# Performance work log

Measured on AMD Instinct MI355X. Metric: run time of the kernel, lower is better.

## Reference

```python
import jax, jax.numpy as jnp
import numpy as np
from jax import lax

NUM_MASK_PARAMS = 67  # 66 weights (64 feat + 2 coord channels) + 1 bias
NUM_GEN_PARAMS = 134


def _coord_maps(h, w, dtype):
    yy = jnp.broadcast_to(jnp.linspace(-1.0, 1.0, h, dtype=dtype)[:, None], (h, w))
    xx = jnp.broadcast_to(jnp.linspace(-1.0, 1.0, w, dtype=dtype)[None, :], (h, w))
    return xx, yy


def _dynamic_head(x_cat, p):
    # x_cat: [66, H, W]; p: [num_ins, 67] -> [num_ins, H, W]
    w = p[:, :NUM_MASK_PARAMS - 1]
    b = p[:, NUM_MASK_PARAMS - 1]
    return jnp.einsum('ic,chw->ihw', w, x_cat) + b[:, None, None]


def setup_inputs() -> dict:
    key = jax.random.key(0)
    ks = jax.random.split(key, 10)
    C, HM, WM, HH, WH, MB, HID = 256, 272, 480, 136, 240, 64, 64
    rn = lambda k, s, sc=1.0: jax.random.normal(k, s, dtype=jnp.float32) * sc
    return {
        'out0': rn(ks[0], (1, C, HM, WM)),
        'out1': rn(ks[1], (1, C, HH, WH)),
        'hm_w': rn(ks[2], (1, C), 0.05),
        'hm_b': jnp.zeros((1,), jnp.float32),
        'params_w': rn(ks[3], (NUM_GEN_PARAMS, C), 0.05),
        'params_b': rn(ks[4], (NUM_GEN_PARAMS,), 0.05),
        'mb_w': rn(ks[5], (MB, C, 3, 3), 0.05),
        'mb_b': jnp.zeros((MB,), jnp.float32),
        'mlp_w1': rn(ks[6], (HM, HID), 0.05),
        'mlp_b1': jnp.zeros((HID,), jnp.float32),
        'mlp_w2': rn(ks[7], (HID, 2), 0.05),
        'mlp_b2': jnp.zeros((2,), jnp.float32),
        'num_ins': 4,
    }


def reference(out0, out1, hm_w, hm_b, params_w, params_b, mb_w, mb_b,
              mlp_w1, mlp_b1, mlp_w2, mlp_b2, num_ins):
    h_mask, w_mask = out0.shape[2], out0.shape[3]
    h_hm, w_hm = out1.shape[2], out1.shape[3]

    # ctnet head: 1x1 convs on the stride-16 feature
    hm = jnp.einsum('kc,bchw->bkhw', hm_w, out1) + hm_b[None, :, None, None]
    params = jnp.einsum('kc,bchw->bkhw', params_w, out1) + params_b[None, :, None, None]
    hm = jnp.clip(jax.nn.sigmoid(hm), 1e-4, 1.0 - 1e-4)  # [1,1,h_hm,w_hm]
    # [1,134,h,w] -> [h*w, 134]
    params_flat = jnp.transpose(params[0], (1, 2, 0)).reshape(-1, NUM_GEN_PARAMS)

    # 3x3 maxpool NMS (stride 1, pad 1), keep only local peaks
    hmax = lax.reduce_window(hm, -jnp.inf, lax.max, (1, 1, 3, 3), (1, 1, 1, 1),
                             [(0, 0), (0, 0), (1, 1), (1, 1)])
    keep = (hmax == hm).astype(hm.dtype)
    heat_nms = (hm * keep).reshape(-1)

    scores, inds = lax.top_k(heat_nms, num_ins)

    # mask branch: 3x3 conv + relu on the stride-8 feature
    mask_branch = lax.conv_general_dilated(out0, mb_w, (1, 1), 'SAME',
                                           dimension_numbers=('NCHW', 'OIHW', 'NCHW'))
    mask_branch = jax.nn.relu(mask_branch + mb_b[None, :, None, None])  # [1,64,H,W]

    xx, yy = _coord_maps(h_mask, w_mask, mask_branch.dtype)
    x_cat = jnp.concatenate([mask_branch[0], xx[None], yy[None]], axis=0)  # [66,H,W]

    gen_params = params_flat[inds]  # [num_ins, 134]
    masks0 = _dynamic_head(x_cat, gen_params[:, :NUM_MASK_PARAMS])   # [num_ins,H,W]
    regs0 = _dynamic_head(x_cat, gen_params[:, NUM_MASK_PARAMS:])    # [num_ins,H,W]

    # row-wise vertical-range MLP over h_mask
    feat_range = jnp.transpose(masks0, (0, 2, 1))  # [num_ins, w_mask, h_mask]
    h1 = jax.nn.relu(feat_range @ mlp_w1 + mlp_b1)
    feat_range = h1 @ mlp_w2 + mlp_b2  # [num_ins, w_mask, 2]

    return scores, inds, regs0, masks0, feat_range
```

## Files before the change

### kernel.cpp

```cpp
#include <hip/hip_runtime.h>
#include <math.h>
#include <limits.h>

#define C_IN 256
#define HM_H 136
#define HM_W 240
#define HM_N (HM_H * HM_W)
#define MB   64
#define MH   272
#define MW   480
#define MN   (MH * MW)
#define NP   134
#define NI   4
#define HID  64

#define REG_OFF   8
#define MASK_OFF  (8 + NI * MN)
#define FEAT_OFF  (8 + 2 * NI * MN)

#define WS_HM   0
#define WS_CV   HM_N
#define WS_CI   (HM_N + 512)
#define WS_GP   (2 * HM_N)
#define WS_WT_F 65824

typedef float  f32x4  __attribute__((ext_vector_type(4)));
typedef short  bf16x8 __attribute__((ext_vector_type(8)));
typedef unsigned short u16x8 __attribute__((ext_vector_type(8)));

__device__ __forceinline__ unsigned short f2bf(float f) {
  unsigned int u = __float_as_uint(f);
  u += 0x7FFFu + ((u >> 16) & 1u);
  return (unsigned short)(u >> 16);
}
__device__ __forceinline__ float b2f(unsigned short h) {
  return __uint_as_float(((unsigned int)h) << 16);
}

__device__ __forceinline__ void glds16(const void* g, void* l) {
  __builtin_amdgcn_global_load_lds(
      (const __attribute__((address_space(1))) unsigned int*)g,
      (__attribute__((address_space(3))) unsigned int*)l, 16, 0, 0);
}

__global__ void k_prep(const float* __restrict__ mb_w, unsigned short* __restrict__ wt,
                       const float* __restrict__ out1, const float* __restrict__ hm_w,
                       const float* __restrict__ hm_b, float* __restrict__ ws_hm) {
  __shared__ float part[4][64];
  if (blockIdx.x < 576) {
    int idx = blockIdx.x * 256 + threadIdx.x;
    int j    = idx & 7;
    int lane = (idx >> 3) & 63;
    int nt   = (idx >> 9) & 3;
    int gt   = idx >> 11;
    int t    = gt % 9;
    int g    = gt / 9;
    int n = nt * 16 + (lane & 15);
    int c = g * 32 + (lane >> 4) * 8 + j;
    wt[idx] = f2bf(mb_w[(n * C_IN + c) * 9 + t]);
  } else {
    int b = blockIdx.x - 576, t = threadIdx.x;
    int cg = t >> 6, pl = t & 63;
    int p = b * 64 + pl;
    float s = 0.f;
    #pragma unroll 16
    for (int c = 0; c < 64; ++c)
      s += hm_w[cg * 64 + c] * out1[(cg * 64 + c) * HM_N + p];
    part[cg][pl] = s;
    __syncthreads();
    if (t < 64) {
      float tot = part[0][t] + part[1][t] + part[2][t] + part[3][t] + hm_b[0];
      float sig = 1.f / (1.f + expf(-tot));
      sig = fminf(fmaxf(sig, 1e-4f), 1.f - 1e-4f);
      ws_hm[b * 64 + t] = sig;
    }
  }
}

__device__ __forceinline__ bool better(float av, int ai, float bv, int bi) {
  return (av > bv) || (av == bv && ai < bi);
}

template<int NTHR>
__device__ void top4_tree(float* sv, int* si, int t) {
  for (int s = NTHR / 2; s >= 1; s >>= 1) {
    if (t < s) {
      float a[4], b[4]; int ai[4], bj[4];
      #pragma unroll
      for (int k = 0; k < 4; ++k) {
        a[k] = sv[t * 4 + k];        ai[k] = si[t * 4 + k];
        b[k] = sv[(t + s) * 4 + k];  bj[k] = si[(t + s) * 4 + k];
      }
      float ov[4]; int oi[4];
      int i = 0, j = 0;
      #pragma unroll
      for (int k = 0; k < 4; ++k) {
        if (better(a[i], ai[i], b[j], bj[j])) { ov[k] = a[i]; oi[k] = ai[i]; ++i; }
        else                                   { ov[k] = b[j]; oi[k] = bj[j]; ++j; }
      }
      #pragma unroll
      for (int k = 0; k < 4; ++k) { sv[t * 4 + k] = ov[k]; si[t * 4 + k] = oi[k]; }
    }
    __syncthreads();
  }
}

__global__ void k_nms_top(const float* __restrict__ ws_hm, float* __restrict__ candv,
                          int* __restrict__ candi) {
  __shared__ float sv[256 * 4];
  __shared__ int   si[256 * 4];
  int b = blockIdx.x, t = threadIdx.x;
  float v = -1.f; int idx = INT_MAX;
  if (t < 255) {
    int p = b * 255 + t;
    int y = p / HM_W, x = p - y * HM_W;
    float c = ws_hm[p], m = c;
    #pragma unroll
    for (int dy = -1; dy <= 1; ++dy)
      #pragma unroll
      for (int dx = -1; dx <= 1; ++dx) {
        int yy = y + dy, xx = x + dx;
        if (yy >= 0 && yy < HM_H && xx >= 0 && xx < HM_W)
          m = fmaxf(m, ws_hm[yy * HM_W + xx]);
      }
    v = (c == m) ? c : 0.f;
    idx = p;
  }
  sv[t * 4] = v; si[t * 4] = idx;
  #pragma unroll
  for (int k = 1; k < 4; ++k) { sv[t * 4 + k] = -1.f; si[t * 4 + k] = INT_MAX; }
  __syncthreads();
  top4_tree<256>(sv, si, t);
  if (t == 0) {
    #pragma unroll
    for (int k = 0; k < 4; ++k) { candv[b * 4 + k] = sv[k]; candi[b * 4 + k] = si[k]; }
  }
}

__global__ void k_gen(const float* __restrict__ candv, const int* __restrict__ candi,
                      const float* __restrict__ out1, const float* __restrict__ params_w,
                      const float* __restrict__ params_b, float* __restrict__ ws_gp,
                      float* __restrict__ d_out) {
  __shared__ float sv[128 * 4];
  __shared__ int   si[128 * 4];
  __shared__ float col[C_IN];
  int t = threadIdx.x, i = blockIdx.x;
  if (t < 128) {
    #pragma unroll
    for (int k = 0; k < 4; ++k) { sv[t * 4 + k] = candv[t * 4 + k]; si[t * 4 + k] = candi[t * 4 + k]; }
  }
  __syncthreads();
  top4_tree<128>(sv, si, t);
  if (i == 0 && t < 4) {
    d_out[t]     = sv[t];
    d_out[4 + t] = (float)si[t];
  }
  int p = si[i];
  col[t] = out1[t * HM_N + p];
  __syncthreads();
  if (t < NP) {
    float s = params_b[t];
    #pragma unroll 8
    for (int c = 0; c < C_IN; ++c) s += params_w[t * C_IN + c] * col[c];
    ws_gp[i * NP + t] = s;
  }
}

#define SR   18
#define RP   36
#define BUFU (SR * RP * 32)
#define WOFF (2 * BUFU)

#define PIPE_BARRIER() do {                                   \
    __builtin_amdgcn_sched_barrier(0);                        \
    asm volatile("s_waitcnt lgkmcnt(0)" ::: "memory");        \
    __builtin_amdgcn_s_barrier();                             \
    __builtin_amdgcn_sched_barrier(0);                        \
  } while (0)

#define STAGE_W3(G, B)                                                    \
  if (wv == 7 && (G) < 24) {                                              \
    const char* wsrc = (const char*)wt + (G) * 12288 + lane * 16;         \
    char* wdst = (char*)smem + 2 * WOFF + (B) * 12288;                    \
    _Pragma("unroll")                                                     \
    for (int i_ = 0; i_ < 12; ++i_)                                       \
      glds16(wsrc + i_ * 1024, wdst + i_ * 1024);                         \
  }

#define MFMA16(A, B, C) __builtin_amdgcn_mfma_f32_16x16x32_bf16(A, B, C, 0, 0, 0)

#define TAPS3(P) {                                                        \
    const unsigned short* wl = smem + WOFF + (P) * 6144 + lane * 8;       \
    _Pragma("unroll")                                                     \
    for (int tt = 0; tt < 3; ++tt) {                                      \
      bf16x8 bb0 = *(const bf16x8*)(wl + tt * 2048);                      \
      bf16x8 bb1 = *(const bf16x8*)(wl + tt * 2048 + 512);                \
      bf16x8 bb2 = *(const bf16x8*)(wl + tt * 2048 + 1024);               \
      bf16x8 bb3 = *(const bf16x8*)(wl + tt * 2048 + 1536);               \
      unsigned pk = lrdp[(P) * 3 + tt];                                   \
      const unsigned short* c0 = cur + (pk & 0xFFFFu);                    \
      const unsigned short* c1 = cur + (pk >> 16);                        \
      bf16x8 a0 = *(const bf16x8*)c0;                                     \
      bf16x8 a1 = *(const bf16x8*)(c0 + 512);                             \
      bf16x8 a2 = *(const bf16x8*)c1;                                     \
      bf16x8 a3 = *(const bf16x8*)(c1 + 512);                             \
      acc[0][0] = MFMA16(a0, bb0, acc[0][0]);                             \
      acc[0][1] = MFMA16(a0, bb1, acc[0][1]);                             \
      acc[0][2] = MFMA16(a0, bb2, acc[0][2]);                             \
      acc[0][3] = MFMA16(a0, bb3, acc[0][3]);                             \
      acc[1][0] = MFMA16(a1, bb0, acc[1][0]);                             \
      acc[1][1] = MFMA16(a1, bb1, acc[1][1]);                             \
      acc[1][2] = MFMA16(a1, bb2, acc[1][2]);                             \
      acc[1][3] = MFMA16(a1, bb3, acc[1][3]);                             \
      acc[2][0] = MFMA16(a2, bb0, acc[2][0]);                             \
      acc[2][1] = MFMA16(a2, bb1, acc[2][1]);                             \
      acc[2][2] = MFMA16(a2, bb2, acc[2][2]);                             \
      acc[2][3] = MFMA16(a2, bb3, acc[2][3]);                             \
      acc[3][0] = MFMA16(a3, bb0, acc[3][0]);                             \
      acc[3][1] = MFMA16(a3, bb1, acc[3][1]);                             \
      acc[3][2] = MFMA16(a3, bb2, acc[3][2]);                             \
      acc[3][3] = MFMA16(a3, bb3, acc[3][3]);                             \
    } }

__device__ __forceinline__ void stage_store8(unsigned short* buf, const f32x4* dq,
                                             bool gv, const int* lw, unsigned sm) {
  #pragma unroll
  for (int e = 0; e < 4; ++e) if ((sm >> e) & 1u) {
    u16x8 v;
    #pragma unroll
    for (int j = 0; j < 8; ++j) v[j] = f2bf(gv ? dq[j][e] : 0.f);
    *(u16x8*)(buf + lw[e]) = v;
  }
}

__global__ __launch_bounds__(512, 2) void k_conv_mfma(
    const float* __restrict__ out0, const unsigned short* __restrict__ wt,
    const float* __restrict__ mb_b, const float* __restrict__ ws_gp,
    float* __restrict__ d_out) {
  __shared__ unsigned short smem[2 * BUFU + 3 * 6144];

  int tid  = threadIdx.x;
  int lane = tid & 63;
  int wv   = tid >> 6;
  int n15  = lane & 15;
  int kq   = lane >> 4;
  int gx0 = blockIdx.x * 32, gy0 = blockIdx.y * 16;

  bool ustage = tid < 360;
  int u    = ustage ? tid : 0;
  int co8  = u / 180;
  int rem  = u - co8 * 180;
  int row  = rem / 10;
  int qx   = rem - row * 10;
  int iy   = gy0 + row - 1;
  int ixq  = gx0 + 4 * qx - 4;
  bool gvld = ustage && (iy >= 0) && (iy < MH) && (ixq >= 0) && (ixq + 3 < MW);
  int goffA = gvld ? (co8 * 8 * MN + iy * MW + ixq) : 0;
  int lwsA[4]; unsigned smask = 0;
  #pragma unroll
  for (int e = 0; e < 4; ++e) {
    int sx = 4 * qx - 3 + e;
    bool sv = ustage && (sx >= 0) && (sx < RP);
    int pixw = row * RP + (sv ? sx : 0);
    int w2 = (pixw ^ (pixw >> 2)) & 3;
    int q  = (pixw ^ row) & 1;
    lwsA[e] = (pixw >> 1) * 64 + ((co8 ^ w2) << 4) + q * 8;
    if (sv) smask |= (1u << e);
  }

  unsigned lrdp[9];
  #pragma unroll
  for (int t = 0; t < 9; ++t) {
    int ty = t / 3, tx = t - ty * 3;
    int sr0 = 2 * wv + ty;
    int pix0 = sr0 * RP + n15 + tx;
    int w20 = (pix0 ^ (pix0 >> 2)) & 3;
    int q0  = (pix0 ^ sr0) & 1;
    unsigned o0 = (pix0 >> 1) * 64 + ((kq ^ w20) << 4) + q0 * 8;
    int sr1 = sr0 + 1;
    int pix1 = sr1 * RP + n15 + tx;
    int w21 = (pix1 ^ (pix1 >> 2)) & 3;
    int q1  = (pix1 ^ sr1) & 1;
    unsigned o1 = (pix1 >> 1) * 64 + ((kq ^ w21) << 4) + q1 * 8;
    lrdp[t] = o0 | (o1 << 16);
  }

  {
    f32x4 dq[8];
    if (ustage) {
      const float* sp = out0 + goffA;
      #pragma unroll
      for (int j = 0; j < 8; ++j) dq[j] = *(const f32x4*)(sp + j * MN);
    }
    stage_store8(smem, dq, gvld, lwsA, smask);
    if (ustage) {
      const float* sp = out0 + goffA + 16 * MN;
      #pragma unroll
      for (int j = 0; j < 8; ++j) dq[j] = *(const f32x4*)(sp + j * MN);
    }
    {
      int lwsB[4];
      #pragma unroll
      for (int e = 0; e < 4; ++e) lwsB[e] = lwsA[e] ^ 32;
      stage_store8(smem, dq, gvld, lwsB, smask);
    }
  }
  __builtin_amdgcn_sched_barrier(0);
  STAGE_W3(0, 0);
  STAGE_W3(1, 1);
  if (wv == 7) asm volatile("s_waitcnt vmcnt(12)" ::: "memory");
  PIPE_BARRIER();

  f32x4 acc[4][4];
  #pragma unroll
  for (int i = 0; i < 4; ++i)
    #pragma unroll
    for (int nt = 0; nt < 4; ++nt)
      acc[i][nt] = (f32x4){0.f, 0.f, 0.f, 0.f};

  #pragma unroll 1
  for (int g = 0; g < 8; ++g) {
    const unsigned short* cur = smem + (g & 1) * BUFU;
    unsigned short*       nxt = smem + ((g + 1) & 1) * BUFU;
    const float*          src = out0 + (g + 1) * (32 * MN);
    f32x4 dq[8];

    STAGE_W3(3 * g + 2, 2);
    if (g < 7 && ustage) {
      const float* sp = src + goffA;
      #pragma unroll
      for (int j = 0; j < 8; ++j) dq[j] = *(const f32x4*)(sp + j * MN);
    }
    __builtin_amdgcn_sched_barrier(0);
    TAPS3(0)
    if (wv == 7) asm volatile("s_waitcnt vmcnt(12)" ::: "memory");
    PIPE_BARRIER();

    STAGE_W3(3 * g + 3, 0);
    if (g < 7) stage_store8(nxt, dq, gvld, lwsA, smask);
    if (g < 7 && ustage) {
      const float* sp = src + goffA + 16 * MN;
      #pragma unroll
      for (int j = 0; j < 8; ++j) dq[j] = *(const f32x4*)(sp + j * MN);
    }
    __builtin_amdgcn_sched_barrier(0);
    TAPS3(1)
    if (wv == 7) {
      if (g == 7) asm volatile("s_waitcnt vmcnt(0)" ::: "memory");
      else        asm volatile("s_waitcnt vmcnt(12)" ::: "memory");
    }
    PIPE_BARRIER();

    STAGE_W3(3 * g + 4, 1);
    if (g < 7) {
      int lwsB[4];
      #pragma unroll
      for (int e = 0; e < 4; ++e) lwsB[e] = lwsA[e] ^ 32;
      stage_store8(nxt, dq, gvld, lwsB, smask);
    }
    __builtin_amdgcn_sched_barrier(0);
    TAPS3(2)
    if (wv == 7) {
      if (g == 7) asm volatile("s_waitcnt vmcnt(0)" ::: "memory");
      else        asm volatile("s_waitcnt vmcnt(12)" ::: "memory");
    }
    PIPE_BARRIER();
  }

  #define ES 66
  {
    float bias[4];
    #pragma unroll
    for (int nt = 0; nt < 4; ++nt) bias[nt] = mb_b[nt * 16 + n15];
    #pragma unroll
    for (int i = 0; i < 4; ++i) {
      int pbase = (2 * wv + (i >> 1)) * 32 + (i & 1) * 16;
      #pragma unroll
      for (int nt = 0; nt < 4; ++nt)
        #pragma unroll
        for (int reg = 0; reg < 4; ++reg) {
          float vv = fmaxf(acc[i][nt][reg] + bias[nt], 0.f);
          smem[(pbase + kq * 4 + reg) * ES + nt * 16 + n15] = f2bf(vv);
        }
    }
  }
  __syncthreads();

  int p = tid & 255, hh = tid >> 8;
  int ob = hh * 32;
  float* pf = (float*)smem + 16896;
  #pragma unroll 1
  for (int ps = 0; ps < 2; ++ps) {
    int pixel = ps * 256 + p;
    float mres[4] = {0.f, 0.f, 0.f, 0.f};
    float rres[4] = {0.f, 0.f, 0.f, 0.f};
    #pragma unroll 8
    for (int o = 0; o < 32; ++o) {
      float v = b2f(smem[pixel * ES + ob + o]);
      #pragma unroll
      for (int i = 0; i < 4; ++i) {
        mres[i] += ws_gp[i * NP + ob + o] * v;
        rres[i] += ws_gp[i * NP + 67 + ob + o] * v;
      }
    }
    if (hh) {
      #pragma unroll
      for (int i = 0; i < 4; ++i) { pf[p * 8 + i] = mres[i]; pf[p * 8 + 4 + i] = rres[i]; }
    }
    __syncthreads();
    if (!hh) {
      int r = pixel >> 5, xcol = pixel & 31;
      int gy = gy0 + r, gx = gx0 + xcol;
      float xc = -1.f + (2.f / 479.f) * (float)gx;
      float yc = -1.f + (2.f / 271.f) * (float)gy;
      int pix = gy * MW + gx;
      #pragma unroll
      for (int i = 0; i < 4; ++i) {
        const float* gp = ws_gp + i * NP;
        d_out[MASK_OFF + i * MN + pix] = mres[i] + pf[p * 8 + i]     + gp[66]  + gp[64]  * xc + gp[65]  * yc;
        d_out[REG_OFF  + i * MN + pix] = rres[i] + pf[p * 8 + 4 + i] + gp[133] + gp[131] * xc + gp[132] * yc;
      }
    }
    __syncthreads();
  }
}

__global__ void k_mlp(const float* __restrict__ masks0, const float* __restrict__ w1,
                      const float* __restrict__ b1, const float* __restrict__ w2,
                      const float* __restrict__ b2, float* __restrict__ d_out) {
  int blk = blockIdx.x;
  int i = blk / MW;
  int w = blk - i * MW;
  int k = threadIdx.x;
  const float* mcol = masks0 + i * MN + w;
  float s = b1[k];
  #pragma unroll 4
  for (int h = 0; h < MH; ++h) s += mcol[h * MW] * w1[h * HID + k];
  s = fmaxf(s, 0.f);
  float o0 = s * w2[k * 2 + 0];
  float o1 = s * w2[k * 2 + 1];
  #pragma unroll
  for (int off = 32; off >= 1; off >>= 1) {
    o0 += __shfl_down(o0, off);
    o1 += __shfl_down(o1, off);
  }
  if (k == 0) {
    d_out[FEAT_OFF + blk * 2 + 0] = o0 + b2[0];
    d_out[FEAT_OFF + blk * 2 + 1] = o1 + b2[1];
  }
}

extern "C" void kernel_launch(void* const* d_in, const int* in_sizes, int n_in,
                              void* d_out, int out_size, void* d_ws, size_t ws_size,
                              hipStream_t stream) {
  const float* out0     = (const float*)d_in[0];
  const float* out1     = (const float*)d_in[1];
  const float* hm_w     = (const float*)d_in[2];
  const float* hm_b     = (const float*)d_in[3];
  const float* params_w = (const float*)d_in[4];
  const float* params_b = (const float*)d_in[5];
  const float* mb_w     = (const float*)d_in[6];
  const float* mb_b     = (const float*)d_in[7];
  const float* mlp_w1   = (const float*)d_in[8];
  const float* mlp_b1   = (const float*)d_in[9];
  const float* mlp_w2   = (const float*)d_in[10];
  const float* mlp_b2   = (const float*)d_in[11];

  float* ws      = (float*)d_ws;
  float* ws_hm   = ws + WS_HM;
  float* candv   = ws + WS_CV;
  int*   candi   = (int*)(ws + WS_CI);
  float* ws_gp   = ws + WS_GP;
  unsigned short* ws_wt = (unsigned short*)(ws + WS_WT_F);
  float* out     = (float*)d_out;

  k_prep<<<1086, 256, 0, stream>>>(mb_w, ws_wt, out1, hm_w, hm_b, ws_hm);
  k_nms_top<<<128, 256, 0, stream>>>(ws_hm, candv, candi);
  k_gen<<<NI, 256, 0, stream>>>(candv, candi, out1, params_w, params_b, ws_gp, out);
  dim3 gconv(MW / 32, MH / 16);
  k_conv_mfma<<<gconv, 512, 0, stream>>>(out0, ws_wt, mb_b, ws_gp, out);
  k_mlp<<<NI * MW, 64, 0, stream>>>(out + MASK_OFF, mlp_w1, mlp_b1, mlp_w2, mlp_b2, out);
}
```

Before: 311.6 us.

## Deepen conv input prefetch to two groups and remap blocks across XCDs

The 3x3 conv kernel now keeps two register sets (dqA/dqB) and prefetches input channels one full group ahead, issuing global loads a whole iteration before the LDS store instead of within the same iteration. This is meant to hide more global-load latency behind the MFMA taps. The 2D grid also becomes a 1D grid of 255 blocks, remapped so that consecutive tiles land on the same XCD (L2 locality for the halo rows). The extra registers may hurt occupancy under launch_bounds(512,2), and the vmcnt waits were not adjusted for the deeper pipeline.

```diff
diff --git a/kernel.cpp b/kernel.cpp
--- a/kernel.cpp
+++ b/kernel.cpp
@@ -244,7 +244,12 @@
   int wv   = tid >> 6;
   int n15  = lane & 15;
   int kq   = lane >> 4;
-  int gx0 = blockIdx.x * 32, gy0 = blockIdx.y * 16;
+
+  int orig = blockIdx.x;
+  int xcd  = orig & 7, pos = orig >> 3;
+  int wgid = (xcd < 7) ? (xcd * 32 + pos) : (224 + pos);
+  int bx = wgid / 17, by = wgid - bx * 17;
+  int gx0 = bx * 32, gy0 = by * 16;
 
   bool ustage = tid < 360;
   int u    = ustage ? tid : 0;
@@ -285,25 +290,32 @@
     lrdp[t] = o0 | (o1 << 16);
   }
 
+  f32x4 dqA[8], dqB[8];
+  if (ustage) {
+    const float* sp = out0 + goffA;
+    #pragma unroll
+    for (int j = 0; j < 8; ++j) dqA[j] = *(const f32x4*)(sp + j * MN);
+  }
+  stage_store8(smem, dqA, gvld, lwsA, smask);
+  if (ustage) {
+    const float* sp = out0 + goffA + 16 * MN;
+    #pragma unroll
+    for (int j = 0; j < 8; ++j) dqB[j] = *(const f32x4*)(sp + j * MN);
+  }
   {
-    f32x4 dq[8];
-    if (ustage) {
-      const float* sp = out0 + goffA;
-      #pragma unroll
-      for (int j = 0; j < 8; ++j) dq[j] = *(const f32x4*)(sp + j * MN);
-    }
-    stage_store8(smem, dq, gvld, lwsA, smask);
-    if (ustage) {
-      const float* sp = out0 + goffA + 16 * MN;
-      #pragma unroll
-      for (int j = 0; j < 8; ++j) dq[j] = *(const f32x4*)(sp + j * MN);
-    }
-    {
-      int lwsB[4];
-      #pragma unroll
-      for (int e = 0; e < 4; ++e) lwsB[e] = lwsA[e] ^ 32;
-      stage_store8(smem, dq, gvld, lwsB, smask);
-    }
+    int lwsB[4];
+    #pragma unroll
+    for (int e = 0; e < 4; ++e) lwsB[e] = lwsA[e] ^ 32;
+    stage_store8(smem, dqB, gvld, lwsB, smask);
+  }
+  __builtin_amdgcn_sched_barrier(0);
+  if (ustage) {
+    const float* sp = out0 + 32 * MN + goffA;
+    #pragma unroll
+    for (int j = 0; j < 8; ++j) dqA[j] = *(const f32x4*)(sp + j * MN);
+    const float* sq = out0 + 32 * MN + goffA + 16 * MN;
+    #pragma unroll
+    for (int j = 0; j < 8; ++j) dqB[j] = *(const f32x4*)(sq + j * MN);
   }
   __builtin_amdgcn_sched_barrier(0);
   STAGE_W3(0, 0);
@@ -322,14 +334,14 @@
   for (int g = 0; g < 8; ++g) {
     const unsigned short* cur = smem + (g & 1) * BUFU;
     unsigned short*       nxt = smem + ((g + 1) & 1) * BUFU;
-    const float*          src = out0 + (g + 1) * (32 * MN);
-    f32x4 dq[8];
 
     STAGE_W3(3 * g + 2, 2);
-    if (g < 7 && ustage) {
-      const float* sp = src + goffA;
-      #pragma unroll
-      for (int j = 0; j < 8; ++j) dq[j] = *(const f32x4*)(sp + j * MN);
+    if (g < 7) stage_store8(nxt, dqA, gvld, lwsA, smask);
+    __builtin_amdgcn_sched_barrier(0);
+    if (g < 6 && ustage) {
+      const float* sp = out0 + (g + 2) * (32 * MN) + goffA;
+      #pragma unroll
+      for (int j = 0; j < 8; ++j) dqA[j] = *(const f32x4*)(sp + j * MN);
     }
     __builtin_amdgcn_sched_barrier(0);
     TAPS3(0)
@@ -337,11 +349,17 @@
     PIPE_BARRIER();
 
     STAGE_W3(3 * g + 3, 0);
-    if (g < 7) stage_store8(nxt, dq, gvld, lwsA, smask);
-    if (g < 7 && ustage) {
-      const float* sp = src + goffA + 16 * MN;
-      #pragma unroll
-      for (int j = 0; j < 8; ++j) dq[j] = *(const f32x4*)(sp + j * MN);
+    if (g < 7) {
+      int lwsB[4];
+      #pragma unroll
+      for (int e = 0; e < 4; ++e) lwsB[e] = lwsA[e] ^ 32;
+      stage_store8(nxt, dqB, gvld, lwsB, smask);
+    }
+    __builtin_amdgcn_sched_barrier(0);
+    if (g < 6 && ustage) {
+      const float* sp = out0 + (g + 2) * (32 * MN) + goffA + 16 * MN;
+      #pragma unroll
+      for (int j = 0; j < 8; ++j) dqB[j] = *(const f32x4*)(sp + j * MN);
     }
     __builtin_amdgcn_sched_barrier(0);
     TAPS3(1)
@@ -352,13 +370,6 @@
     PIPE_BARRIER();
 
     STAGE_W3(3 * g + 4, 1);
-    if (g < 7) {
-      int lwsB[4];
-      #pragma unroll
-      for (int e = 0; e < 4; ++e) lwsB[e] = lwsA[e] ^ 32;
-      stage_store8(nxt, dq, gvld, lwsB, smask);
-    }
-    __builtin_amdgcn_sched_barrier(0);
     TAPS3(2)
     if (wv == 7) {
       if (g == 7) asm volatile("s_waitcnt vmcnt(0)" ::: "memory");
@@ -477,7 +488,6 @@
   k_prep<<<1086, 256, 0, stream>>>(mb_w, ws_wt, out1, hm_w, hm_b, ws_hm);
   k_nms_top<<<128, 256, 0, stream>>>(ws_hm, candv, candi);
   k_gen<<<NI, 256, 0, stream>>>(candv, candi, out1, params_w, params_b, ws_gp, out);
-  dim3 gconv(MW / 32, MH / 16);
-  k_conv_mfma<<<gconv, 512, 0, stream>>>(out0, ws_wt, mb_b, ws_gp, out);
+  k_conv_mfma<<<255, 512, 0, stream>>>(out0, ws_wt, mb_b, ws_gp, out);
   k_mlp<<<NI * MW, 64, 0, stream>>>(out + MASK_OFF, mlp_w1, mlp_b1, mlp_w2, mlp_b2, out);
 }
```

After: 307.2 us. No clear change (-1.4%).
